# Performance work log

Hardware: AMD Instinct MI355X
Metric: run time of the kernel (lower is better)

## Reference

```python
import jax, jax.numpy as jnp
import numpy as np

N_NODES = 50000


def setup_inputs() -> dict:
    key = jax.random.key(0)
    k1, k2, k3, k4, k5 = jax.random.split(key, 5)
    x = jax.random.normal(k1, (N_NODES, 256), dtype=jnp.float32)
    edge_row = jax.random.randint(k2, (800000,), 0, N_NODES, dtype=jnp.int32)
    edge_col = jax.random.randint(k3, (800000,), 0, N_NODES, dtype=jnp.int32)
    edge_val = jax.random.uniform(k4, (800000,), dtype=jnp.float32)
    W = jax.random.normal(k5, (256, 256), dtype=jnp.float32) * 0.0625  # ~1/sqrt(256)
    b = jnp.zeros((256,), dtype=jnp.float32)
    return {"x": x, "edge_row": edge_row, "edge_col": edge_col,
            "edge_val": edge_val, "W": W, "b": b}


def reference(x, edge_row, edge_col, edge_val, W, b):
    # SpMM: agg[i] = sum_{e: row(e)=i} val(e) * x[col(e)]
    msgs = edge_val[:, None] * x[edge_col]                      # [E, F_in]
    agg = jax.ops.segment_sum(msgs, edge_row, num_segments=N_NODES)  # [N, F_in]
    # nn.Linear: agg @ W.T + b
    return jnp.einsum('nf,of->no', agg, W) + b
```

## Files before the change

kernel.cpp:

```cpp
#include <hip/hip_runtime.h>

typedef unsigned short u16;
typedef __attribute__((ext_vector_type(8))) short short8;
typedef __attribute__((ext_vector_type(4))) float f32x4;
typedef __attribute__((ext_vector_type(4))) u16 u16x4;

#define F 256

__device__ __forceinline__ u16 f2bf(float f) {
  unsigned u = __float_as_uint(f);
  unsigned r = u + 0x7fffu + ((u >> 16) & 1u);
  return (u16)(r >> 16);
}

__device__ __forceinline__ f32x4 bf4_to_f32(u16x4 u) {
  f32x4 x;
#pragma unroll
  for (int j = 0; j < 4; j++) x[j] = __uint_as_float((unsigned)u[j] << 16);
  return x;
}

__device__ __forceinline__ void gemm_body(const float* __restrict__ x,
                                          const float* __restrict__ Wm,
                                          u16* __restrict__ yb,
                                          int NT, int gidx, int stride) {
  int w = (int)(threadIdx.x >> 6);
  int lane = threadIdx.x & 63;
  int ln = lane & 15, q = lane >> 4;

  short8 Bf[4][8];
#pragma unroll
  for (int j = 0; j < 4; j++) {
#pragma unroll
    for (int t = 0; t < 8; t++) {
      const f32x4* wp = (const f32x4*)(Wm + (size_t)((4 * w + j) * 16 + ln) * F + t * 32 + q * 8);
      f32x4 wlo = wp[0], whi = wp[1];
      short8 bfrag;
#pragma unroll
      for (int i = 0; i < 4; i++) {
        bfrag[i]     = (short)f2bf(wlo[i]);
        bfrag[4 + i] = (short)f2bf(whi[i]);
      }
      Bf[j][t] = bfrag;
    }
  }

  for (int mt = gidx; mt < NT; mt += stride) {
    const float* arow = x + (size_t)(mt * 16 + ln) * F + q * 8;
    f32x4 acc[4];
#pragma unroll
    for (int j = 0; j < 4; j++) acc[j] = (f32x4){0.f, 0.f, 0.f, 0.f};

#pragma unroll
    for (int t = 0; t < 8; t++) {
      const f32x4* a4 = (const f32x4*)(arow + t * 32);
      f32x4 alo = a4[0], ahi = a4[1];
      short8 a;
#pragma unroll
      for (int j = 0; j < 4; j++) {
        a[j]     = (short)f2bf(alo[j]);
        a[4 + j] = (short)f2bf(ahi[j]);
      }
#pragma unroll
      for (int j = 0; j < 4; j++) {
        acc[j] = __builtin_amdgcn_mfma_f32_16x16x32_bf16(a, Bf[j][t], acc[j], 0, 0, 0);
      }
    }

    int m0 = mt * 16;
#pragma unroll
    for (int j = 0; j < 4; j++) {
#pragma unroll
      for (int r = 0; r < 4; r++) {
        yb[(size_t)(m0 + q * 4 + r) * F + (4 * w + j) * 16 + ln] = f2bf(acc[j][r]);
      }
    }
  }
}

__global__ void __launch_bounds__(256, 1) gemmzero_k(const float* __restrict__ x,
                                                     const float* __restrict__ Wm,
                                                     u16* __restrict__ yb,
                                                     int NT, int stride,
                                                     int4* __restrict__ zp, int zeroN4) {
  int tid = blockIdx.x * 256 + (int)threadIdx.x;
  for (int i = tid; i < zeroN4; i += stride * 256) zp[i] = make_int4(0, 0, 0, 0);
  gemm_body(x, Wm, yb, NT, blockIdx.x, stride);
}

__global__ void __launch_bounds__(256) scatter_k(const int* __restrict__ erow,
                                                 const int* __restrict__ ecol,
                                                 const float* __restrict__ eval,
                                                 int* __restrict__ curp,
                                                 int2* __restrict__ epk, int E, int CAP) {
  int e = blockIdx.x * 256 + (int)threadIdx.x;
  if (e < E) {
    int r = erow[e];
    int p = atomicAdd(&curp[r << 4], 1);
    if (p < CAP) epk[(size_t)r * CAP + p] = make_int2(ecol[e], __float_as_int(eval[e]));
  }
}

__global__ void __launch_bounds__(256) gather_dir_k(const int* __restrict__ curp,
                                                    const int2* __restrict__ epk,
                                                    const u16* __restrict__ yb,
                                                    const float* __restrict__ bias,
                                                    float* __restrict__ out, int NN) {
  int wave = (int)((blockIdx.x * 256 + threadIdx.x) >> 6);
  int lane = threadIdx.x & 63;
  if (wave >= NN) return;
  int deg = curp[wave << 4];
  if (deg > 64) deg = 64;

  int2 m = epk[(size_t)wave * 64 + lane];
  int mc = m.x, mv = m.y;
  const u16* ybl = yb + lane * 4;

  f32x4 acc0 = ((const f32x4*)bias)[lane];
  f32x4 acc1 = (f32x4){0.f, 0.f, 0.f, 0.f};
  f32x4 acc2 = (f32x4){0.f, 0.f, 0.f, 0.f};
  f32x4 acc3 = (f32x4){0.f, 0.f, 0.f, 0.f};

  int k = 0;
  for (; k + 8 <= deg; k += 8) {
    int c0 = __shfl(mc, k + 0), c1 = __shfl(mc, k + 1);
    int c2 = __shfl(mc, k + 2), c3 = __shfl(mc, k + 3);
    int c4 = __shfl(mc, k + 4), c5 = __shfl(mc, k + 5);
    int c6 = __shfl(mc, k + 6), c7 = __shfl(mc, k + 7);
    u16x4 u0 = *(const u16x4*)(ybl + (size_t)c0 * F);
    u16x4 u1 = *(const u16x4*)(ybl + (size_t)c1 * F);
    u16x4 u2 = *(const u16x4*)(ybl + (size_t)c2 * F);
    u16x4 u3 = *(const u16x4*)(ybl + (size_t)c3 * F);
    u16x4 u4 = *(const u16x4*)(ybl + (size_t)c4 * F);
    u16x4 u5 = *(const u16x4*)(ybl + (size_t)c5 * F);
    u16x4 u6 = *(const u16x4*)(ybl + (size_t)c6 * F);
    u16x4 u7 = *(const u16x4*)(ybl + (size_t)c7 * F);
    float v0 = __int_as_float(__shfl(mv, k + 0)), v1 = __int_as_float(__shfl(mv, k + 1));
    float v2 = __int_as_float(__shfl(mv, k + 2)), v3 = __int_as_float(__shfl(mv, k + 3));
    float v4 = __int_as_float(__shfl(mv, k + 4)), v5 = __int_as_float(__shfl(mv, k + 5));
    float v6 = __int_as_float(__shfl(mv, k + 6)), v7 = __int_as_float(__shfl(mv, k + 7));
    acc0 += v0 * bf4_to_f32(u0);
    acc1 += v1 * bf4_to_f32(u1);
    acc2 += v2 * bf4_to_f32(u2);
    acc3 += v3 * bf4_to_f32(u3);
    acc0 += v4 * bf4_to_f32(u4);
    acc1 += v5 * bf4_to_f32(u5);
    acc2 += v6 * bf4_to_f32(u6);
    acc3 += v7 * bf4_to_f32(u7);
  }
  for (; k < deg; k++) {
    int c = __shfl(mc, k);
    float v = __int_as_float(__shfl(mv, k));
    u16x4 u = *(const u16x4*)(ybl + (size_t)c * F);
    acc0 += v * bf4_to_f32(u);
  }
  acc0 += acc1;
  acc2 += acc3;
  acc0 += acc2;
  ((f32x4*)out)[(size_t)wave * 64 + lane] = acc0;
}


__global__ void hist_k(const int* __restrict__ erow, int* __restrict__ off, int E) {
  int e = blockIdx.x * 256 + threadIdx.x;
  if (e < E) atomicAdd(&off[erow[e] + 1], 1);
}

__global__ void scanA_k(int* __restrict__ a, int* __restrict__ blks, int n) {
  __shared__ int s[256];
  int t = threadIdx.x;
  int i = blockIdx.x * 256 + t;
  s[t] = (i < n) ? a[i] : 0;
  __syncthreads();
  for (int d = 1; d < 256; d <<= 1) {
    int v = (t >= d) ? s[t - d] : 0;
    __syncthreads();
    s[t] += v;
    __syncthreads();
  }
  if (i < n) a[i] = s[t];
  if (t == 255) blks[blockIdx.x] = s[255];
}

__global__ void scanB_k(int* __restrict__ a, const int* __restrict__ blks,
                        int* __restrict__ cur, int n, int nn, int nb) {
  __shared__ int s[256];
  int t = threadIdx.x;
  s[t] = (t < nb) ? blks[t] : 0;
  __syncthreads();
  for (int d = 1; d < 256; d <<= 1) {
    int v = (t >= d) ? s[t - d] : 0;
    __syncthreads();
    s[t] += v;
    __syncthreads();
  }
  int prefix = (blockIdx.x == 0) ? 0 : s[blockIdx.x - 1];
  int i = blockIdx.x * 256 + t;
  if (i < n) {
    int v = a[i] + prefix;
    a[i] = v;
    if (i < nn) cur[i] = v;
  }
}

__global__ void scatter_csr_k(const int* __restrict__ erow, const int* __restrict__ ecol,
                              const float* __restrict__ eval, int* __restrict__ cur,
                              int2* __restrict__ epk, int E) {
  int e = blockIdx.x * 256 + threadIdx.x;
  if (e < E) {
    int r = erow[e];
    int p = atomicAdd(&cur[r], 1);
    epk[p] = make_int2(ecol[e], __float_as_int(eval[e]));
  }
}

__global__ void __launch_bounds__(256) gather_csr_k(const int* __restrict__ off,
                                                    const int2* __restrict__ epk,
                                                    const u16* __restrict__ yb,
                                                    const float* __restrict__ bias,
                                                    float* __restrict__ out, int NN) {
  int wave = (int)((blockIdx.x * 256 + threadIdx.x) >> 6);
  int lane = threadIdx.x & 63;
  if (wave >= NN) return;
  int s = off[wave], e = off[wave + 1];

  f32x4 acc0 = ((const f32x4*)bias)[lane];
  f32x4 acc1 = (f32x4){0.f, 0.f, 0.f, 0.f};
  f32x4 acc2 = (f32x4){0.f, 0.f, 0.f, 0.f};
  f32x4 acc3 = (f32x4){0.f, 0.f, 0.f, 0.f};

  int k = s;
  for (; k + 4 <= e; k += 4) {
    int2 p0 = epk[k], p1 = epk[k + 1], p2 = epk[k + 2], p3 = epk[k + 3];
    u16x4 u0 = *(const u16x4*)(yb + (size_t)p0.x * F + lane * 4);
    u16x4 u1 = *(const u16x4*)(yb + (size_t)p1.x * F + lane * 4);
    u16x4 u2 = *(const u16x4*)(yb + (size_t)p2.x * F + lane * 4);
    u16x4 u3 = *(const u16x4*)(yb + (size_t)p3.x * F + lane * 4);
    acc0 += __int_as_float(p0.y) * bf4_to_f32(u0);
    acc1 += __int_as_float(p1.y) * bf4_to_f32(u1);
    acc2 += __int_as_float(p2.y) * bf4_to_f32(u2);
    acc3 += __int_as_float(p3.y) * bf4_to_f32(u3);
  }
  for (; k < e; k++) {
    int2 p = epk[k];
    u16x4 u = *(const u16x4*)(yb + (size_t)p.x * F + lane * 4);
    acc0 += __int_as_float(p.y) * bf4_to_f32(u);
  }
  acc0 += acc1;
  acc2 += acc3;
  acc0 += acc2;
  ((f32x4*)out)[(size_t)wave * 64 + lane] = acc0;
}

__global__ void __launch_bounds__(256, 1) gemm_only_k(const float* __restrict__ x,
                                                      const float* __restrict__ Wm,
                                                      u16* __restrict__ yb, int NT, int stride) {
  gemm_body(x, Wm, yb, NT, blockIdx.x, stride);
}

extern "C" void kernel_launch(void* const* d_in, const int* in_sizes, int n_in,
                              void* d_out, int out_size, void* d_ws, size_t ws_size,
                              hipStream_t stream) {
  const float* x    = (const float*)d_in[0];
  const int*   erow = (const int*)d_in[1];
  const int*   ecol = (const int*)d_in[2];
  const float* eval = (const float*)d_in[3];
  const float* Wm   = (const float*)d_in[4];
  const float* bias = (const float*)d_in[5];
  float* out = (float*)d_out;

  int NN = in_sizes[0] / F;
  int E  = in_sizes[1];

  char* base = (char*)d_ws;
  size_t o = 0;
  auto carve = [&](size_t bytes) {
    void* p = base + o;
    o += (bytes + 255) & ~(size_t)255;
    return p;
  };
  u16* yb   = (u16*)carve((size_t)NN * F * 2);
  int* curp = (int*)carve((size_t)NN * 64);

  size_t avail = (ws_size > o) ? (ws_size - o) : 0;
  size_t capmax = avail / ((size_t)NN * 8);
  int CAP = 64;

  int NT = (NN + 15) / 16;

  if (capmax >= 64) {
    int2* epk = (int2*)carve((size_t)NN * CAP * 8);
    int nBlocks = 512;
    int zeroN4 = NN * 16 / 4;
    gemmzero_k<<<nBlocks, 256, 0, stream>>>(x, Wm, yb, NT, nBlocks, (int4*)curp, zeroN4);
    scatter_k<<<(E + 255) / 256, 256, 0, stream>>>(erow, ecol, eval, curp, epk, E, CAP);
    gather_dir_k<<<(NN + 3) / 4, 256, 0, stream>>>(curp, epk, yb, bias, out, NN);
  } else {
    int*  cur  = curp;
    int*  off  = (int*)carve((size_t)(NN + 1) * 4);
    int*  blks = (int*)carve(256 * 4);
    int2* epk  = (int2*)carve((size_t)E * 8);
    int nOff = NN + 1;
    int nbOff = (nOff + 255) / 256;
    int nbE = (E + 255) / 256;
    hipMemsetAsync(off, 0, (size_t)nOff * 4, stream);
    hist_k<<<nbE, 256, 0, stream>>>(erow, off, E);
    scanA_k<<<nbOff, 256, 0, stream>>>(off, blks, nOff);
    scanB_k<<<nbOff, 256, 0, stream>>>(off, blks, cur, nOff, NN, nbOff);
    scatter_csr_k<<<nbE, 256, 0, stream>>>(erow, ecol, eval, cur, epk, E);
    gemm_only_k<<<512, 256, 0, stream>>>(x, Wm, yb, NT, 512);
    gather_csr_k<<<(NN + 3) / 4, 256, 0, stream>>>(off, epk, yb, bias, out, NN);
  }
}
```

Baseline: 241.6 us.

## Fuse GEMM and edge scatter into one kernel with block specialization

Merges the GEMM-plus-zeroing kernel and the scatter kernel into one launch of 4096 blocks. Every eighth block runs a GEMM tile and the rest grid-stride over edges doing the atomic bucket insert, so the GEMM and the scatter can run at the same time. Zeroing of the counters moves to a hipMemsetAsync before the launch. The gather kernel now loads packed edge entries only for lanes below the degree rounded up to eight, which skips reads of unused slots. The risk is that GEMM and scatter blocks compete for compute units, and the split assumes the fixed counts of 512 GEMM blocks and 3584 scatter blocks.

```diff
diff --git a/kernel.cpp b/kernel.cpp
--- a/kernel.cpp
+++ b/kernel.cpp
@@ -78,26 +78,25 @@
   }
 }
 
-__global__ void __launch_bounds__(256, 1) gemmzero_k(const float* __restrict__ x,
+__global__ void __launch_bounds__(256, 1) gemmscat_k(const float* __restrict__ x,
                                                      const float* __restrict__ Wm,
-                                                     u16* __restrict__ yb,
-                                                     int NT, int stride,
-                                                     int4* __restrict__ zp, int zeroN4) {
-  int tid = blockIdx.x * 256 + (int)threadIdx.x;
-  for (int i = tid; i < zeroN4; i += stride * 256) zp[i] = make_int4(0, 0, 0, 0);
-  gemm_body(x, Wm, yb, NT, blockIdx.x, stride);
-}
-
-__global__ void __launch_bounds__(256) scatter_k(const int* __restrict__ erow,
-                                                 const int* __restrict__ ecol,
-                                                 const float* __restrict__ eval,
-                                                 int* __restrict__ curp,
-                                                 int2* __restrict__ epk, int E, int CAP) {
-  int e = blockIdx.x * 256 + (int)threadIdx.x;
-  if (e < E) {
-    int r = erow[e];
-    int p = atomicAdd(&curp[r << 4], 1);
-    if (p < CAP) epk[(size_t)r * CAP + p] = make_int2(ecol[e], __float_as_int(eval[e]));
+                                                     u16* __restrict__ yb, int NT,
+                                                     const int* __restrict__ erow,
+                                                     const int* __restrict__ ecol,
+                                                     const float* __restrict__ eval,
+                                                     int* __restrict__ curp,
+                                                     int2* __restrict__ epk,
+                                                     int E, int CAP) {
+  int bid = (int)blockIdx.x;
+  if ((bid & 7) == 0) {
+    gemm_body(x, Wm, yb, NT, bid >> 3, 512);
+  } else {
+    int sid = bid - (bid >> 3) - 1;
+    for (int e = sid * 256 + (int)threadIdx.x; e < E; e += 3584 * 256) {
+      int r = erow[e];
+      int p = atomicAdd(&curp[r << 4], 1);
+      if (p < CAP) epk[(size_t)r * CAP + p] = make_int2(ecol[e], __float_as_int(eval[e]));
+    }
   }
 }
 
@@ -111,9 +110,14 @@
   if (wave >= NN) return;
   int deg = curp[wave << 4];
   if (deg > 64) deg = 64;
-
-  int2 m = epk[(size_t)wave * 64 + lane];
-  int mc = m.x, mv = m.y;
+  int degr = (deg + 7) & ~7;
+
+  int mc = 0, mv = 0;
+  if (lane < degr) {
+    int2 m = epk[(size_t)wave * 64 + lane];
+    mc = m.x;
+    mv = m.y;
+  }
   const u16* ybl = yb + lane * 4;
 
   f32x4 acc0 = ((const f32x4*)bias)[lane];
@@ -290,10 +294,8 @@
 
   if (capmax >= 64) {
     int2* epk = (int2*)carve((size_t)NN * CAP * 8);
-    int nBlocks = 512;
-    int zeroN4 = NN * 16 / 4;
-    gemmzero_k<<<nBlocks, 256, 0, stream>>>(x, Wm, yb, NT, nBlocks, (int4*)curp, zeroN4);
-    scatter_k<<<(E + 255) / 256, 256, 0, stream>>>(erow, ecol, eval, curp, epk, E, CAP);
+    hipMemsetAsync(curp, 0, (size_t)NN * 64, stream);
+    gemmscat_k<<<4096, 256, 0, stream>>>(x, Wm, yb, NT, erow, ecol, eval, curp, epk, E, CAP);
     gather_dir_k<<<(NN + 3) / 4, 256, 0, stream>>>(curp, epk, yb, bias, out, NN);
   } else {
     int*  cur  = curp;
```

Measured after the change: 589.3 us. +143.9%, slower.

## Store GEMM output feature-blocked and gather per 32-feature block for cache locality

Applied to the files above, without the earlier changes.

The bf16 GEMM output is rewritten in a feature-blocked layout, eight blocks of 32 features, each laid out node-major. A new gather kernel assigns each block to one feature slice, so 8 lanes handle a node and a workgroup covers 32 nodes. Each feature slice of yb is then about 3.2 MB and can stay cache-resident during the random row gathers. The fused zeroing in the GEMM is replaced by a hipMemsetAsync, and the GEMM grid grows from 512 to 768 blocks. In exchange, each node's edge list is re-read once per feature block, and the gather inner loop gains per-edge degree predication.

```diff
diff --git a/kernel.cpp b/kernel.cpp
--- a/kernel.cpp
+++ b/kernel.cpp
@@ -23,7 +23,7 @@
 __device__ __forceinline__ void gemm_body(const float* __restrict__ x,
                                           const float* __restrict__ Wm,
                                           u16* __restrict__ yb,
-                                          int NT, int gidx, int stride) {
+                                          int NT, int NN, int gidx, int stride) {
   int w = (int)(threadIdx.x >> 6);
   int lane = threadIdx.x & 63;
   int ln = lane & 15, q = lane >> 4;
@@ -70,22 +70,21 @@
     int m0 = mt * 16;
 #pragma unroll
     for (int j = 0; j < 4; j++) {
+      int fb = 2 * w + (j >> 1);
+      int fi = ((j & 1) << 4) + ln;
 #pragma unroll
       for (int r = 0; r < 4; r++) {
-        yb[(size_t)(m0 + q * 4 + r) * F + (4 * w + j) * 16 + ln] = f2bf(acc[j][r]);
-      }
-    }
-  }
-}
-
-__global__ void __launch_bounds__(256, 1) gemmzero_k(const float* __restrict__ x,
-                                                     const float* __restrict__ Wm,
-                                                     u16* __restrict__ yb,
-                                                     int NT, int stride,
-                                                     int4* __restrict__ zp, int zeroN4) {
-  int tid = blockIdx.x * 256 + (int)threadIdx.x;
-  for (int i = tid; i < zeroN4; i += stride * 256) zp[i] = make_int4(0, 0, 0, 0);
-  gemm_body(x, Wm, yb, NT, blockIdx.x, stride);
+        yb[((size_t)fb * NN + (m0 + q * 4 + r)) * 32 + fi] = f2bf(acc[j][r]);
+      }
+    }
+  }
+}
+
+__global__ void __launch_bounds__(256, 1) gemm_only_k(const float* __restrict__ x,
+                                                      const float* __restrict__ Wm,
+                                                      u16* __restrict__ yb, int NT, int NN,
+                                                      int stride) {
+  gemm_body(x, Wm, yb, NT, NN, blockIdx.x, stride);
 }
 
 __global__ void __launch_bounds__(256) scatter_k(const int* __restrict__ erow,
@@ -101,63 +100,50 @@
   }
 }
 
-__global__ void __launch_bounds__(256) gather_dir_k(const int* __restrict__ curp,
-                                                    const int2* __restrict__ epk,
-                                                    const u16* __restrict__ yb,
-                                                    const float* __restrict__ bias,
-                                                    float* __restrict__ out, int NN) {
-  int wave = (int)((blockIdx.x * 256 + threadIdx.x) >> 6);
-  int lane = threadIdx.x & 63;
-  if (wave >= NN) return;
-  int deg = curp[wave << 4];
+__global__ void __launch_bounds__(256) gather_fb_k(const int* __restrict__ curp,
+                                                   const int2* __restrict__ epk,
+                                                   const u16* __restrict__ yb,
+                                                   const float* __restrict__ bias,
+                                                   float* __restrict__ out, int NN) {
+  int bid = (int)blockIdx.x;
+  int fb = bid & 7;
+  int nblk = bid >> 3;
+  int t = (int)threadIdx.x;
+  int g = t >> 3;
+  int l8 = t & 7;
+  int lw = (t & 63) & ~7;
+  int node = nblk * 32 + g;
+  if (node >= NN) return;
+
+  int deg = curp[node << 4];
   if (deg > 64) deg = 64;
 
-  int2 m = epk[(size_t)wave * 64 + lane];
-  int mc = m.x, mv = m.y;
-  const u16* ybl = yb + lane * 4;
-
-  f32x4 acc0 = ((const f32x4*)bias)[lane];
+  const u16* yfb = yb + (size_t)fb * NN * 32 + l8 * 4;
+  const int2* mrow = epk + (size_t)node * 64;
+
+  f32x4 acc0 = ((const f32x4*)bias)[fb * 8 + l8];
   f32x4 acc1 = (f32x4){0.f, 0.f, 0.f, 0.f};
-  f32x4 acc2 = (f32x4){0.f, 0.f, 0.f, 0.f};
-  f32x4 acc3 = (f32x4){0.f, 0.f, 0.f, 0.f};
-
-  int k = 0;
-  for (; k + 8 <= deg; k += 8) {
-    int c0 = __shfl(mc, k + 0), c1 = __shfl(mc, k + 1);
-    int c2 = __shfl(mc, k + 2), c3 = __shfl(mc, k + 3);
-    int c4 = __shfl(mc, k + 4), c5 = __shfl(mc, k + 5);
-    int c6 = __shfl(mc, k + 6), c7 = __shfl(mc, k + 7);
-    u16x4 u0 = *(const u16x4*)(ybl + (size_t)c0 * F);
-    u16x4 u1 = *(const u16x4*)(ybl + (size_t)c1 * F);
-    u16x4 u2 = *(const u16x4*)(ybl + (size_t)c2 * F);
-    u16x4 u3 = *(const u16x4*)(ybl + (size_t)c3 * F);
-    u16x4 u4 = *(const u16x4*)(ybl + (size_t)c4 * F);
-    u16x4 u5 = *(const u16x4*)(ybl + (size_t)c5 * F);
-    u16x4 u6 = *(const u16x4*)(ybl + (size_t)c6 * F);
-    u16x4 u7 = *(const u16x4*)(ybl + (size_t)c7 * F);
-    float v0 = __int_as_float(__shfl(mv, k + 0)), v1 = __int_as_float(__shfl(mv, k + 1));
-    float v2 = __int_as_float(__shfl(mv, k + 2)), v3 = __int_as_float(__shfl(mv, k + 3));
-    float v4 = __int_as_float(__shfl(mv, k + 4)), v5 = __int_as_float(__shfl(mv, k + 5));
-    float v6 = __int_as_float(__shfl(mv, k + 6)), v7 = __int_as_float(__shfl(mv, k + 7));
-    acc0 += v0 * bf4_to_f32(u0);
-    acc1 += v1 * bf4_to_f32(u1);
-    acc2 += v2 * bf4_to_f32(u2);
-    acc3 += v3 * bf4_to_f32(u3);
-    acc0 += v4 * bf4_to_f32(u4);
-    acc1 += v5 * bf4_to_f32(u5);
-    acc2 += v6 * bf4_to_f32(u6);
-    acc3 += v7 * bf4_to_f32(u7);
-  }
-  for (; k < deg; k++) {
-    int c = __shfl(mc, k);
-    float v = __int_as_float(__shfl(mv, k));
-    u16x4 u = *(const u16x4*)(ybl + (size_t)c * F);
-    acc0 += v * bf4_to_f32(u);
+
+  for (int k = 0; k < deg; k += 8) {
+    int2 m = mrow[k + l8];
+#pragma unroll
+    for (int j = 0; j < 8; j += 2) {
+      if (k + j < deg) {
+        int c0 = __shfl(m.x, lw + j);
+        float v0 = __int_as_float(__shfl(m.y, lw + j));
+        u16x4 u0 = *(const u16x4*)(yfb + (size_t)c0 * 32);
+        acc0 += v0 * bf4_to_f32(u0);
+      }
+      if (k + j + 1 < deg) {
+        int c1 = __shfl(m.x, lw + j + 1);
+        float v1 = __int_as_float(__shfl(m.y, lw + j + 1));
+        u16x4 u1 = *(const u16x4*)(yfb + (size_t)c1 * 32);
+        acc1 += v1 * bf4_to_f32(u1);
+      }
+    }
   }
   acc0 += acc1;
-  acc2 += acc3;
-  acc0 += acc2;
-  ((f32x4*)out)[(size_t)wave * 64 + lane] = acc0;
+  ((f32x4*)(out + (size_t)node * 256 + fb * 32))[l8] = acc0;
 }
 
 
@@ -224,38 +210,27 @@
   if (wave >= NN) return;
   int s = off[wave], e = off[wave + 1];
 
+  size_t fbbase = (size_t)(lane >> 3) * NN;
+  int fi = (lane & 7) * 4;
+
   f32x4 acc0 = ((const f32x4*)bias)[lane];
   f32x4 acc1 = (f32x4){0.f, 0.f, 0.f, 0.f};
-  f32x4 acc2 = (f32x4){0.f, 0.f, 0.f, 0.f};
-  f32x4 acc3 = (f32x4){0.f, 0.f, 0.f, 0.f};
 
   int k = s;
-  for (; k + 4 <= e; k += 4) {
-    int2 p0 = epk[k], p1 = epk[k + 1], p2 = epk[k + 2], p3 = epk[k + 3];
-    u16x4 u0 = *(const u16x4*)(yb + (size_t)p0.x * F + lane * 4);
-    u16x4 u1 = *(const u16x4*)(yb + (size_t)p1.x * F + lane * 4);
-    u16x4 u2 = *(const u16x4*)(yb + (size_t)p2.x * F + lane * 4);
-    u16x4 u3 = *(const u16x4*)(yb + (size_t)p3.x * F + lane * 4);
+  for (; k + 2 <= e; k += 2) {
+    int2 p0 = epk[k], p1 = epk[k + 1];
+    u16x4 u0 = *(const u16x4*)(yb + (fbbase + p0.x) * 32 + fi);
+    u16x4 u1 = *(const u16x4*)(yb + (fbbase + p1.x) * 32 + fi);
     acc0 += __int_as_float(p0.y) * bf4_to_f32(u0);
     acc1 += __int_as_float(p1.y) * bf4_to_f32(u1);
-    acc2 += __int_as_float(p2.y) * bf4_to_f32(u2);
-    acc3 += __int_as_float(p3.y) * bf4_to_f32(u3);
   }
   for (; k < e; k++) {
     int2 p = epk[k];
-    u16x4 u = *(const u16x4*)(yb + (size_t)p.x * F + lane * 4);
+    u16x4 u = *(const u16x4*)(yb + (fbbase + p.x) * 32 + fi);
     acc0 += __int_as_float(p.y) * bf4_to_f32(u);
   }
   acc0 += acc1;
-  acc2 += acc3;
-  acc0 += acc2;
   ((f32x4*)out)[(size_t)wave * 64 + lane] = acc0;
-}
-
-__global__ void __launch_bounds__(256, 1) gemm_only_k(const float* __restrict__ x,
-                                                      const float* __restrict__ Wm,
-                                                      u16* __restrict__ yb, int NT, int stride) {
-  gemm_body(x, Wm, yb, NT, blockIdx.x, stride);
 }
 
 extern "C" void kernel_launch(void* const* d_in, const int* in_sizes, int n_in,
@@ -290,11 +265,11 @@
 
   if (capmax >= 64) {
     int2* epk = (int2*)carve((size_t)NN * CAP * 8);
-    int nBlocks = 512;
-    int zeroN4 = NN * 16 / 4;
-    gemmzero_k<<<nBlocks, 256, 0, stream>>>(x, Wm, yb, NT, nBlocks, (int4*)curp, zeroN4);
+    hipMemsetAsync(curp, 0, (size_t)NN * 64, stream);
     scatter_k<<<(E + 255) / 256, 256, 0, stream>>>(erow, ecol, eval, curp, epk, E, CAP);
-    gather_dir_k<<<(NN + 3) / 4, 256, 0, stream>>>(curp, epk, yb, bias, out, NN);
+    gemm_only_k<<<768, 256, 0, stream>>>(x, Wm, yb, NT, NN, 768);
+    int nblkN = (NN + 31) / 32;
+    gather_fb_k<<<nblkN * 8, 256, 0, stream>>>(curp, epk, yb, bias, out, NN);
   } else {
     int*  cur  = curp;
     int*  off  = (int*)carve((size_t)(NN + 1) * 4);
@@ -308,7 +283,7 @@
     scanA_k<<<nbOff, 256, 0, stream>>>(off, blks, nOff);
     scanB_k<<<nbOff, 256, 0, stream>>>(off, blks, cur, nOff, NN, nbOff);
     scatter_csr_k<<<nbE, 256, 0, stream>>>(erow, ecol, eval, cur, epk, E);
-    gemm_only_k<<<512, 256, 0, stream>>>(x, Wm, yb, NT, 512);
+    gemm_only_k<<<768, 256, 0, stream>>>(x, Wm, yb, NT, NN, 768);
     gather_csr_k<<<(NN + 3) / 4, 256, 0, stream>>>(off, epk, yb, bias, out, NN);
   }
 }
```

Measured after the change: 270.7 us. 12.1% more time.

## Stage bf16 weights in swizzled shared memory for GEMM with 512-thread blocks

Applied to the files above, without the earlier changes.

The fused zero+GEMM kernel now converts the whole 256x256 weight matrix to bf16 once per block into a 128KB XOR-swizzled LDS buffer, instead of each wave holding 32 B-fragments in registers. Blocks grow to 512 threads (8 waves, each computing 2 output column tiles), and the grid shrinks to 256 blocks. This is meant to cut register pressure and redundant per-wave global weight loads, at the cost of LDS reads in the inner loop and one block per CU due to LDS size. The old gemm_body is kept for the fallback path.

```diff
diff --git a/kernel.cpp b/kernel.cpp
--- a/kernel.cpp
+++ b/kernel.cpp
@@ -2,10 +2,13 @@
 
 typedef unsigned short u16;
 typedef __attribute__((ext_vector_type(8))) short short8;
+typedef __attribute__((ext_vector_type(8))) u16 u16x8;
 typedef __attribute__((ext_vector_type(4))) float f32x4;
 typedef __attribute__((ext_vector_type(4))) u16 u16x4;
 
 #define F 256
+#define GB 256
+#define GT 512
 
 __device__ __forceinline__ u16 f2bf(float f) {
   unsigned u = __float_as_uint(f);
@@ -20,36 +23,41 @@
   return x;
 }
 
-__device__ __forceinline__ void gemm_body(const float* __restrict__ x,
-                                          const float* __restrict__ Wm,
-                                          u16* __restrict__ yb,
-                                          int NT, int gidx, int stride) {
+__global__ void __launch_bounds__(GT, 1) gemmzero_k(const float* __restrict__ x,
+                                                    const float* __restrict__ Wm,
+                                                    u16* __restrict__ yb, int NT,
+                                                    int4* __restrict__ zp, int zeroN4) {
+  int tid = (int)blockIdx.x * GT + (int)threadIdx.x;
+  for (int i = tid; i < zeroN4; i += GB * GT) zp[i] = make_int4(0, 0, 0, 0);
+
+  __shared__ u16 Bs[F * F];
+
+  for (int ch = (int)threadIdx.x; ch < F * 32; ch += GT) {
+    int r = ch >> 5, cc = ch & 31;
+    const f32x4* wp = (const f32x4*)(Wm + (size_t)r * F + cc * 8);
+    f32x4 lo = wp[0], hi = wp[1];
+    u16x8 v;
+#pragma unroll
+    for (int i = 0; i < 4; i++) {
+      v[i]     = f2bf(lo[i]);
+      v[4 + i] = f2bf(hi[i]);
+    }
+    unsigned sw = (unsigned)(r * 512 + cc * 16) ^ (unsigned)((r & 7) << 4);
+    *(u16x8*)((char*)Bs + sw) = v;
+  }
+  __syncthreads();
+
   int w = (int)(threadIdx.x >> 6);
   int lane = threadIdx.x & 63;
   int ln = lane & 15, q = lane >> 4;
-
-  short8 Bf[4][8];
-#pragma unroll
-  for (int j = 0; j < 4; j++) {
-#pragma unroll
-    for (int t = 0; t < 8; t++) {
-      const f32x4* wp = (const f32x4*)(Wm + (size_t)((4 * w + j) * 16 + ln) * F + t * 32 + q * 8);
-      f32x4 wlo = wp[0], whi = wp[1];
-      short8 bfrag;
-#pragma unroll
-      for (int i = 0; i < 4; i++) {
-        bfrag[i]     = (short)f2bf(wlo[i]);
-        bfrag[4 + i] = (short)f2bf(whi[i]);
-      }
-      Bf[j][t] = bfrag;
-    }
-  }
-
-  for (int mt = gidx; mt < NT; mt += stride) {
+  int row0 = (2 * w) * 16 + ln;
+  const char* bsl = (const char*)Bs;
+  unsigned swl = (unsigned)((ln & 7) << 4);
+
+  for (int mt = (int)blockIdx.x; mt < NT; mt += GB) {
     const float* arow = x + (size_t)(mt * 16 + ln) * F + q * 8;
-    f32x4 acc[4];
-#pragma unroll
-    for (int j = 0; j < 4; j++) acc[j] = (f32x4){0.f, 0.f, 0.f, 0.f};
+    f32x4 acc0 = (f32x4){0.f, 0.f, 0.f, 0.f};
+    f32x4 acc1 = (f32x4){0.f, 0.f, 0.f, 0.f};
 
 #pragma unroll
     for (int t = 0; t < 8; t++) {
@@ -61,31 +69,20 @@
         a[j]     = (short)f2bf(alo[j]);
         a[4 + j] = (short)f2bf(ahi[j]);
       }
-#pragma unroll
-      for (int j = 0; j < 4; j++) {
-        acc[j] = __builtin_amdgcn_mfma_f32_16x16x32_bf16(a, Bf[j][t], acc[j], 0, 0, 0);
-      }
+      unsigned sb = ((unsigned)(t * 64 + q * 16)) ^ swl;
+      short8 b0 = *(const short8*)(bsl + row0 * 512 + sb);
+      short8 b1 = *(const short8*)(bsl + (row0 + 16) * 512 + sb);
+      acc0 = __builtin_amdgcn_mfma_f32_16x16x32_bf16(a, b0, acc0, 0, 0, 0);
+      acc1 = __builtin_amdgcn_mfma_f32_16x16x32_bf16(a, b1, acc1, 0, 0, 0);
     }
 
     int m0 = mt * 16;
 #pragma unroll
-    for (int j = 0; j < 4; j++) {
-#pragma unroll
-      for (int r = 0; r < 4; r++) {
-        yb[(size_t)(m0 + q * 4 + r) * F + (4 * w + j) * 16 + ln] = f2bf(acc[j][r]);
-      }
-    }
-  }
-}
-
-__global__ void __launch_bounds__(256, 1) gemmzero_k(const float* __restrict__ x,
-                                                     const float* __restrict__ Wm,
-                                                     u16* __restrict__ yb,
-                                                     int NT, int stride,
-                                                     int4* __restrict__ zp, int zeroN4) {
-  int tid = blockIdx.x * 256 + (int)threadIdx.x;
-  for (int i = tid; i < zeroN4; i += stride * 256) zp[i] = make_int4(0, 0, 0, 0);
-  gemm_body(x, Wm, yb, NT, blockIdx.x, stride);
+    for (int r = 0; r < 4; r++) {
+      yb[(size_t)(m0 + q * 4 + r) * F + (2 * w) * 16 + ln]       = f2bf(acc0[r]);
+      yb[(size_t)(m0 + q * 4 + r) * F + (2 * w + 1) * 16 + ln]   = f2bf(acc1[r]);
+    }
+  }
 }
 
 __global__ void __launch_bounds__(256) scatter_k(const int* __restrict__ erow,
@@ -161,6 +158,64 @@
 }
 
 
+__device__ __forceinline__ void gemm_body(const float* __restrict__ x,
+                                          const float* __restrict__ Wm,
+                                          u16* __restrict__ yb,
+                                          int NT, int gidx, int stride) {
+  int w = (int)(threadIdx.x >> 6);
+  int lane = threadIdx.x & 63;
+  int ln = lane & 15, q = lane >> 4;
+
+  short8 Bf[4][8];
+#pragma unroll
+  for (int j = 0; j < 4; j++) {
+#pragma unroll
+    for (int t = 0; t < 8; t++) {
+      const f32x4* wp = (const f32x4*)(Wm + (size_t)((4 * w + j) * 16 + ln) * F + t * 32 + q * 8);
+      f32x4 wlo = wp[0], whi = wp[1];
+      short8 bfrag;
+#pragma unroll
+      for (int i = 0; i < 4; i++) {
+        bfrag[i]     = (short)f2bf(wlo[i]);
+        bfrag[4 + i] = (short)f2bf(whi[i]);
+      }
+      Bf[j][t] = bfrag;
+    }
+  }
+
+  for (int mt = gidx; mt < NT; mt += stride) {
+    const float* arow = x + (size_t)(mt * 16 + ln) * F + q * 8;
+    f32x4 acc[4];
+#pragma unroll
+    for (int j = 0; j < 4; j++) acc[j] = (f32x4){0.f, 0.f, 0.f, 0.f};
+
+#pragma unroll
+    for (int t = 0; t < 8; t++) {
+      const f32x4* a4 = (const f32x4*)(arow + t * 32);
+      f32x4 alo = a4[0], ahi = a4[1];
+      short8 a;
+#pragma unroll
+      for (int j = 0; j < 4; j++) {
+        a[j]     = (short)f2bf(alo[j]);
+        a[4 + j] = (short)f2bf(ahi[j]);
+      }
+#pragma unroll
+      for (int j = 0; j < 4; j++) {
+        acc[j] = __builtin_amdgcn_mfma_f32_16x16x32_bf16(a, Bf[j][t], acc[j], 0, 0, 0);
+      }
+    }
+
+    int m0 = mt * 16;
+#pragma unroll
+    for (int j = 0; j < 4; j++) {
+#pragma unroll
+      for (int r = 0; r < 4; r++) {
+        yb[(size_t)(m0 + q * 4 + r) * F + (4 * w + j) * 16 + ln] = f2bf(acc[j][r]);
+      }
+    }
+  }
+}
+
 __global__ void hist_k(const int* __restrict__ erow, int* __restrict__ off, int E) {
   int e = blockIdx.x * 256 + threadIdx.x;
   if (e < E) atomicAdd(&off[erow[e] + 1], 1);
@@ -290,9 +345,8 @@
 
   if (capmax >= 64) {
     int2* epk = (int2*)carve((size_t)NN * CAP * 8);
-    int nBlocks = 512;
     int zeroN4 = NN * 16 / 4;
-    gemmzero_k<<<nBlocks, 256, 0, stream>>>(x, Wm, yb, NT, nBlocks, (int4*)curp, zeroN4);
+    gemmzero_k<<<GB, GT, 0, stream>>>(x, Wm, yb, NT, (int4*)curp, zeroN4);
     scatter_k<<<(E + 255) / 256, 256, 0, stream>>>(erow, ecol, eval, curp, epk, E, CAP);
     gather_dir_k<<<(NN + 3) / 4, 256, 0, stream>>>(curp, epk, yb, bias, out, NN);
   } else {
```

Result: slower. 252.3 us (+4.4%).
